# Kernel tuning notes

Measured on AMD Instinct MI355X. Metric: run time of the kernel, lower is better.

The kernel has to match this reference:

```python
import jax, jax.numpy as jnp
import numpy as np

N_HEADS = 16
HEAD_DIM = 64
D_MODEL = 1024

def setup_inputs() -> dict:
    key = jax.random.key(0)
    k1, k2, k3 = jax.random.split(key, 3)
    B, S = 4, 2048
    x = jax.random.normal(k1, (B, S, D_MODEL), dtype=jnp.float32)
    Wqkv = jax.random.normal(k2, (D_MODEL, 3 * D_MODEL), dtype=jnp.float32) * (D_MODEL ** -0.5)
    bqkv = jnp.zeros((3 * D_MODEL,), dtype=jnp.float32)
    Wo = jax.random.normal(k3, (D_MODEL, D_MODEL), dtype=jnp.float32) * (D_MODEL ** -0.5)
    bo = jnp.zeros((D_MODEL,), dtype=jnp.float32)
    return {"x": x, "Wqkv": Wqkv, "bqkv": bqkv, "Wo": Wo, "bo": bo}

def reference(x, Wqkv, bqkv, Wo, bo):
    B, S, E = x.shape
    H, D = N_HEADS, HEAD_DIM
    qkv = x @ Wqkv + bqkv                      # [B,S,3E]
    q, k, v = jnp.split(qkv, 3, axis=-1)
    q = q.reshape(B, S, H, D).transpose(0, 2, 1, 3)  # [B,H,S,D]
    k = k.reshape(B, S, H, D).transpose(0, 2, 1, 3)
    v = v.reshape(B, S, H, D).transpose(0, 2, 1, 3)
    scores = jnp.einsum('bhsd,bhtd->bhst', q, k) / jnp.sqrt(jnp.float32(D))
    causal = jnp.tril(jnp.ones((S, S), dtype=bool))
    scores = jnp.where(causal[None, None], scores, jnp.float32(-jnp.inf))
    attn = jax.nn.softmax(scores, axis=-1)
    y = jnp.einsum('bhst,bhtd->bhsd', attn, v)       # [B,H,S,D]
    y = y.transpose(0, 2, 1, 3).reshape(B, S, E)
    return y @ Wo + bo
```

## Files before the change

kernel.cpp:

```cpp
#include <hip/hip_runtime.h>
#include <hip/hip_bf16.h>
#include <stdint.h>

typedef __bf16 bf16;
typedef __bf16 bf16x8 __attribute__((ext_vector_type(8)));
typedef __bf16 bf16x4 __attribute__((ext_vector_type(4)));
typedef float  f32x4  __attribute__((ext_vector_type(4)));
typedef float  f32x16 __attribute__((ext_vector_type(16)));

__device__ __forceinline__ void load_lds16(const void* g, void* l) {
  __builtin_amdgcn_global_load_lds((const __attribute__((address_space(1))) void*)g,
                                   (__attribute__((address_space(3))) void*)l, 16, 0, 0);
}

__device__ __forceinline__ unsigned pk2(float a, float b) {
  union { bf16 h[2]; unsigned u; } t;
  t.h[0] = (bf16)a; t.h[1] = (bf16)b;
  return t.u;
}

__global__ __launch_bounds__(256) void f32_to_bf16_k(const float* __restrict__ in,
                                                     bf16* __restrict__ out) {
  int i = (blockIdx.x * 256 + threadIdx.x) * 8;
  float4 a = *(const float4*)(in + i);
  float4 b = *(const float4*)(in + i + 4);
  bf16x8 o;
  o[0] = (bf16)a.x; o[1] = (bf16)a.y; o[2] = (bf16)a.z; o[3] = (bf16)a.w;
  o[4] = (bf16)b.x; o[5] = (bf16)b.y; o[6] = (bf16)b.z; o[7] = (bf16)b.w;
  *(bf16x8*)(out + i) = o;
}

__global__ __launch_bounds__(256) void transpose_to_bf16_k(const float* __restrict__ in,
                                                           bf16* __restrict__ out,
                                                           int K, int N) {
  __shared__ __align__(16) bf16 tile[64 * 72];
  int n0 = blockIdx.x * 64, k0 = blockIdx.y * 64;
  int t = threadIdx.x;
  int r = t >> 2, cq = (t & 3) * 16;
  const float* src = in + (size_t)(k0 + r) * N + n0 + cq;
#pragma unroll
  for (int j = 0; j < 16; j += 4) {
    float4 v = *(const float4*)(src + j);
    tile[r * 72 + cq + j + 0] = (bf16)v.x;
    tile[r * 72 + cq + j + 1] = (bf16)v.y;
    tile[r * 72 + cq + j + 2] = (bf16)v.z;
    tile[r * 72 + cq + j + 3] = (bf16)v.w;
  }
  __syncthreads();
  bf16x8 r0, r1;
#pragma unroll
  for (int j = 0; j < 8; ++j) r0[j] = tile[(cq + j) * 72 + r];
#pragma unroll
  for (int j = 0; j < 8; ++j) r1[j] = tile[(cq + 8 + j) * 72 + r];
  bf16* dst = out + (size_t)(n0 + r) * K + k0 + cq;
  *(bf16x8*)(dst) = r0;
  *(bf16x8*)(dst + 8) = r1;
}

template <int EPI>
__global__ __launch_bounds__(256) void gemm_bt(const bf16* __restrict__ A,
                                               const bf16* __restrict__ BT,
                                               const float* __restrict__ bias,
                                               float* __restrict__ Cf,
                                               bf16* __restrict__ qk,
                                               bf16* __restrict__ vt,
                                               int M, int N, int K) {
  __shared__ __align__(16) bf16 As[128 * 64];
  __shared__ __align__(16) bf16 Bs[128 * 64];
  const int tid = threadIdx.x;
  const int w = tid >> 6, l = tid & 63;
  const int g = l >> 4, c = l & 15;
  const int wm = w >> 1, wn = w & 1;
  const int brow = blockIdx.y * 128;
  const int bcol = blockIdx.x * 128;
  const int lr = l >> 3;
  const int lg = l & 7;

  f32x4 acc[4][4];
#pragma unroll
  for (int m = 0; m < 4; ++m)
#pragma unroll
    for (int n = 0; n < 4; ++n) acc[m][n] = f32x4{0.f, 0.f, 0.f, 0.f};

  const int nkt = K >> 6;
  for (int kt = 0; kt < nkt; ++kt) {
    if (kt) __syncthreads();
    const int k0 = kt * 64;
#pragma unroll
    for (int i = 0; i < 4; ++i) {
      int row = w * 32 + i * 8 + lr;
      int src_k = k0 + ((lg ^ (row & 7)) * 8);
      load_lds16(A + (size_t)(brow + row) * K + src_k, &As[(w * 32 + i * 8) * 64]);
      load_lds16(BT + (size_t)(bcol + row) * K + src_k, &Bs[(w * 32 + i * 8) * 64]);
    }
    asm volatile("s_waitcnt vmcnt(0)" ::: "memory");
    __syncthreads();

#pragma unroll
    for (int ks = 0; ks < 2; ++ks) {
      bf16x8 af[4], bfr[4];
#pragma unroll
      for (int m = 0; m < 4; ++m)
        af[m] = *(const bf16x8*)&As[(wm * 64 + m * 16 + c) * 64 + (((ks * 4 + g) ^ (c & 7)) * 8)];
#pragma unroll
      for (int n = 0; n < 4; ++n)
        bfr[n] = *(const bf16x8*)&Bs[(wn * 64 + n * 16 + c) * 64 + (((ks * 4 + g) ^ (c & 7)) * 8)];
#pragma unroll
      for (int m = 0; m < 4; ++m)
#pragma unroll
        for (int n = 0; n < 4; ++n)
          acc[m][n] = __builtin_amdgcn_mfma_f32_16x16x32_bf16(af[m], bfr[n], acc[m][n], 0, 0, 0);
    }
  }

#pragma unroll
  for (int m = 0; m < 4; ++m) {
    int row_l = wm * 64 + m * 16 + (l >> 4) * 4;
#pragma unroll
    for (int n = 0; n < 4; ++n) {
      int col = bcol + wn * 64 + n * 16 + c;
      float bv = bias[col];
      if (EPI == 0) {
        if (bcol < 2048) {
#pragma unroll
          for (int r = 0; r < 4; ++r) {
            int row = brow + row_l + r;
            qk[(size_t)row * 2048 + col] = (bf16)(acc[m][n][r] + bv);
          }
        } else {
          int hh = (col - 2048) >> 6, dd = (col - 2048) & 63;
          int row0 = brow + row_l;
          int bb = row0 >> 11, ss = row0 & 2047;
          bf16x4 pk;
#pragma unroll
          for (int r = 0; r < 4; ++r) pk[r] = (bf16)(acc[m][n][r] + bv);
          *(bf16x4*)&vt[((size_t)(bb * 16 + hh) * 64 + dd) * 2048 + ss] = pk;
        }
      } else {
#pragma unroll
        for (int r = 0; r < 4; ++r) {
          int row = brow + row_l + r;
          Cf[(size_t)row * N + col] = acc[m][n][r] + bv;
        }
      }
    }
  }
}

__global__ __launch_bounds__(128) void attn_k(const bf16* __restrict__ qkbuf,
                                              const bf16* __restrict__ vtbuf,
                                              bf16* __restrict__ aout) {
  __shared__ __align__(16) bf16 Ks[2][64 * 64];
  __shared__ __align__(16) bf16 Vs[2][64 * 64];

  const int tid = threadIdx.x;
  const int w = tid >> 6, l = tid & 63;
  const int c32 = l & 31, hi = l >> 5;

  const int bid = blockIdx.x;
  const int xcd = bid & 7;
  const int idx = bid >> 3;
  const int bh = xcd * 8 + (idx >> 4);
  const int j = idx & 15;
  const int p = j >> 1, h0 = j & 1;
  const int b = bh >> 4, h = bh & 15;

  const bf16* ksrc = qkbuf + (size_t)(b * 2048) * 2048 + 1024 + h * 64;
  const bf16* vsrc = vtbuf + (size_t)(bh * 64) * 2048;

#pragma unroll 1
  for (int item = 0; item < 2; ++item) {
    const int qblk = item == 0 ? 15 - p : p;
    const int half = item == 0 ? h0 : 1 - h0;
    const int nt = 2 * qblk + half + 1;
    const int qw = qblk * 128 + half * 64 + w * 32;
    const int myq = qw + c32;

    const size_t qoff = (size_t)(b * 2048 + myq) * 2048 + h * 64;
    bf16x8 qf[4];
#pragma unroll
    for (int t = 0; t < 4; ++t) {
      bf16x8 v = *(const bf16x8*)&qkbuf[qoff + t * 16 + hi * 8];
#pragma unroll
      for (int jj = 0; jj < 8; ++jj) v[jj] = (bf16)((float)v[jj] * 0.125f);
      qf[t] = v;
    }

    float m_r = -1e30f, l_r = 0.f;
    f32x16 o[2];
    o[0] = (f32x16)(0.f); o[1] = (f32x16)(0.f);

#define STAGE_TILE(buf, KV0)                                                        \
    {                                                                               \
      const int kv0s = (KV0);                                                       \
      _Pragma("unroll")                                                             \
      for (int i = 0; i < 4; ++i) {                                                 \
        int rr = w * 32 + i * 8 + (l >> 3);                                         \
        int sw = ((l & 7) ^ (rr & 7)) * 8;                                          \
        load_lds16(ksrc + (size_t)(kv0s + rr) * 2048 + sw,                          \
                   &Ks[buf][(w * 32 + i * 8) * 64]);                                \
        load_lds16(vsrc + (size_t)rr * 2048 + kv0s + sw,                            \
                   &Vs[buf][(w * 32 + i * 8) * 64]);                                \
      }                                                                             \
    }

    STAGE_TILE(0, 0)
    asm volatile("s_waitcnt vmcnt(0)" ::: "memory");
    __syncthreads();

    int cur = 0;
    for (int kt = 0; kt < nt; ++kt) {
      const int kv0 = kt * 64;
      if (kt + 1 < nt) STAGE_TILE(cur ^ 1, kv0 + 64)

      const bf16* kb = &Ks[cur][0];
      const bf16* vb = &Vs[cur][0];

      f32x16 st[2];
      st[0] = (f32x16)(0.f); st[1] = (f32x16)(0.f);
      __builtin_amdgcn_s_setprio(1);
#pragma unroll
      for (int t = 0; t < 4; ++t) {
#pragma unroll
        for (int ks = 0; ks < 2; ++ks) {
          int kv = ks * 32 + c32;
          bf16x8 kf = *(const bf16x8*)&kb[kv * 64 + (((2 * t + hi) ^ (kv & 7)) * 8)];
          st[ks] = __builtin_amdgcn_mfma_f32_32x32x16_bf16(kf, qf[t], st[ks], 0, 0, 0);
        }
      }
      __builtin_amdgcn_s_setprio(0);

      if (kv0 + 63 > qw) {
#pragma unroll
        for (int ks = 0; ks < 2; ++ks)
#pragma unroll
          for (int r = 0; r < 16; ++r) {
            int kvidx = kv0 + ks * 32 + (r & 3) + 8 * (r >> 2) + 4 * hi;
            if (kvidx > myq) st[ks][r] = -1e30f;
          }
      }

      float t0[8];
#pragma unroll
      for (int i = 0; i < 8; ++i)
        t0[i] = fmaxf(fmaxf(st[0][i], st[0][i + 8]), fmaxf(st[1][i], st[1][i + 8]));
      float mx = fmaxf(fmaxf(fmaxf(t0[0], t0[1]), fmaxf(t0[2], t0[3])),
                       fmaxf(fmaxf(t0[4], t0[5]), fmaxf(t0[6], t0[7])));
      mx = fmaxf(mx, __shfl_xor(mx, 32, 64));

      if (__any(mx > m_r + 8.0f)) {
        float mn = fmaxf(m_r, mx);
        float al = __expf(m_r - mn);
        m_r = mn;
        l_r *= al;
#pragma unroll
        for (int ds = 0; ds < 2; ++ds)
#pragma unroll
          for (int r = 0; r < 16; ++r) o[ds][r] *= al;
      }

      float s0 = 0.f, s1 = 0.f, s2 = 0.f, s3 = 0.f;
#pragma unroll
      for (int ks = 0; ks < 2; ++ks)
#pragma unroll
        for (int r = 0; r < 16; r += 4) {
          float p0 = __expf(st[ks][r + 0] - m_r);
          float p1 = __expf(st[ks][r + 1] - m_r);
          float p2 = __expf(st[ks][r + 2] - m_r);
          float p3 = __expf(st[ks][r + 3] - m_r);
          st[ks][r + 0] = p0; st[ks][r + 1] = p1;
          st[ks][r + 2] = p2; st[ks][r + 3] = p3;
          s0 += p0; s1 += p1; s2 += p2; s3 += p3;
        }
      float ps = (s0 + s1) + (s2 + s3);
      ps += __shfl_xor(ps, 32, 64);
      l_r += ps;

      bf16x8 pfr[4];
#pragma unroll
      for (int t = 0; t < 4; ++t) {
        const int ks = t >> 1, eb = (t & 1) * 8;
        unsigned we0 = pk2(st[ks][eb + 0], st[ks][eb + 1]);
        unsigned we1 = pk2(st[ks][eb + 2], st[ks][eb + 3]);
        unsigned wo0 = pk2(st[ks][eb + 4], st[ks][eb + 5]);
        unsigned wo1 = pk2(st[ks][eb + 6], st[ks][eb + 7]);
        unsigned v0 = hi ? we0 : wo0;
        unsigned v1 = hi ? we1 : wo1;
        unsigned r0 = __shfl_xor(v0, 32, 64);
        unsigned r1 = __shfl_xor(v1, 32, 64);
        union { unsigned u[4]; bf16x8 v; } pf;
        pf.u[0] = hi ? r0 : we0;
        pf.u[1] = hi ? r1 : we1;
        pf.u[2] = hi ? wo0 : r0;
        pf.u[3] = hi ? wo1 : r1;
        pfr[t] = pf.v;
      }

      __builtin_amdgcn_s_setprio(1);
#pragma unroll
      for (int t = 0; t < 4; ++t) {
#pragma unroll
        for (int ds = 0; ds < 2; ++ds) {
          int d = ds * 32 + c32;
          bf16x8 vf = *(const bf16x8*)&vb[d * 64 + (((2 * t + hi) ^ (d & 7)) * 8)];
          o[ds] = __builtin_amdgcn_mfma_f32_32x32x16_bf16(vf, pfr[t], o[ds], 0, 0, 0);
        }
      }
      __builtin_amdgcn_s_setprio(0);

      asm volatile("s_waitcnt vmcnt(0)" ::: "memory");
      __syncthreads();
      cur ^= 1;
    }

    const float inv = 1.0f / l_r;
    bf16* orow = aout + (size_t)(b * 2048 + myq) * 1024 + h * 64;
#pragma unroll
    for (int ds = 0; ds < 2; ++ds)
#pragma unroll
      for (int rg = 0; rg < 4; ++rg) {
        bf16x4 pk;
#pragma unroll
        for (int i = 0; i < 4; ++i) pk[i] = (bf16)(o[ds][rg * 4 + i] * inv);
        *(bf16x4*)&orow[ds * 32 + rg * 8 + hi * 4] = pk;
      }
#undef STAGE_TILE
  }
}

extern "C" void kernel_launch(void* const* d_in, const int* in_sizes, int n_in,
                              void* d_out, int out_size, void* d_ws, size_t ws_size,
                              hipStream_t stream) {
  const float* x    = (const float*)d_in[0];
  const float* Wqkv = (const float*)d_in[1];
  const float* bqkv = (const float*)d_in[2];
  const float* Wo   = (const float*)d_in[3];
  const float* bo   = (const float*)d_in[4];
  float* out = (float*)d_out;

  char* ws = (char*)d_ws;
  bf16* xb   = (bf16*)(ws);
  bf16* wqt  = (bf16*)(ws + 16777216);
  bf16* wot  = (bf16*)(ws + 23068672);
  bf16* qkb  = (bf16*)(ws + 25165824);
  bf16* vtb  = (bf16*)(ws + 58720256);
  bf16* aob  = (bf16*)(ws + 75497472);

  f32_to_bf16_k<<<dim3(4096), dim3(256), 0, stream>>>(x, xb);
  transpose_to_bf16_k<<<dim3(48, 16), dim3(256), 0, stream>>>(Wqkv, wqt, 1024, 3072);
  transpose_to_bf16_k<<<dim3(16, 16), dim3(256), 0, stream>>>(Wo, wot, 1024, 1024);
  gemm_bt<0><<<dim3(24, 64), dim3(256), 0, stream>>>(xb, wqt, bqkv, nullptr, qkb, vtb,
                                                     8192, 3072, 1024);
  attn_k<<<dim3(1024), dim3(128), 0, stream>>>(qkb, vtb, aob);
  gemm_bt<1><<<dim3(8, 64), dim3(256), 0, stream>>>(aob, wot, bo, out, nullptr, nullptr,
                                                    8192, 1024, 1024);
}
```

Baseline: 194.2 us.

## Split attention into single-wave blocks per 32-query tile without double buffering

Rewrites the attention kernel so each 64-thread block (one wavefront) handles one 32-query tile. The launch goes from 1024 two-wave blocks, each processing two paired query blocks, to 4096 single-wave blocks ordered longest-first. Double-buffered LDS staging and __syncthreads are replaced by a single buffer loaded synchronously each iteration. This removes barriers, halves LDS per block and relies on many resident blocks for latency hiding. In exchange, each block reloads full K/V tiles alone, so K/V traffic per query doubles, and loads no longer overlap compute within a block.

New measurement: 221.1 us. +13.8%, slower.

```diff
diff --git a/kernel.cpp b/kernel.cpp
--- a/kernel.cpp
+++ b/kernel.cpp
@@ -147,185 +147,161 @@
   }
 }
 
-__global__ __launch_bounds__(128) void attn_k(const bf16* __restrict__ qkbuf,
-                                              const bf16* __restrict__ vtbuf,
-                                              bf16* __restrict__ aout) {
-  __shared__ __align__(16) bf16 Ks[2][64 * 64];
-  __shared__ __align__(16) bf16 Vs[2][64 * 64];
-
-  const int tid = threadIdx.x;
-  const int w = tid >> 6, l = tid & 63;
+__global__ __launch_bounds__(64) void attn_k(const bf16* __restrict__ qkbuf,
+                                             const bf16* __restrict__ vtbuf,
+                                             bf16* __restrict__ aout) {
+  __shared__ __align__(16) bf16 Ks[64 * 64];
+  __shared__ __align__(16) bf16 Vs[64 * 64];
+
+  const int l = threadIdx.x;
   const int c32 = l & 31, hi = l >> 5;
 
   const int bid = blockIdx.x;
   const int xcd = bid & 7;
-  const int idx = bid >> 3;
-  const int bh = xcd * 8 + (idx >> 4);
-  const int j = idx & 15;
-  const int p = j >> 1, h0 = j & 1;
+  const int u = bid >> 3;
+  const int bh = xcd * 8 + (u >> 6);
+  const int qb = 63 - (u & 63);
   const int b = bh >> 4, h = bh & 15;
+  const int q0 = qb * 32;
+  const int nt = (qb >> 1) + 1;
+  const int myq = q0 + c32;
 
   const bf16* ksrc = qkbuf + (size_t)(b * 2048) * 2048 + 1024 + h * 64;
   const bf16* vsrc = vtbuf + (size_t)(bh * 64) * 2048;
 
-#pragma unroll 1
-  for (int item = 0; item < 2; ++item) {
-    const int qblk = item == 0 ? 15 - p : p;
-    const int half = item == 0 ? h0 : 1 - h0;
-    const int nt = 2 * qblk + half + 1;
-    const int qw = qblk * 128 + half * 64 + w * 32;
-    const int myq = qw + c32;
-
-    const size_t qoff = (size_t)(b * 2048 + myq) * 2048 + h * 64;
-    bf16x8 qf[4];
+  const size_t qoff = (size_t)(b * 2048 + myq) * 2048 + h * 64;
+  bf16x8 qf[4];
+#pragma unroll
+  for (int t = 0; t < 4; ++t) {
+    bf16x8 v = *(const bf16x8*)&qkbuf[qoff + t * 16 + hi * 8];
+#pragma unroll
+    for (int j = 0; j < 8; ++j) v[j] = (bf16)((float)v[j] * 0.125f);
+    qf[t] = v;
+  }
+
+  float m_r = -1e30f, l_r = 0.f;
+  f32x16 o[2];
+  o[0] = (f32x16)(0.f); o[1] = (f32x16)(0.f);
+
+  for (int kt = 0; kt < nt; ++kt) {
+    const int kv0 = kt * 64;
+
+    asm volatile("s_waitcnt lgkmcnt(0)" ::: "memory");
+    __builtin_amdgcn_sched_barrier(0);
+#pragma unroll
+    for (int i = 0; i < 8; ++i) {
+      int row = i * 8 + (l >> 3);
+      int sw = ((l & 7) ^ (row & 7)) * 8;
+      load_lds16(ksrc + (size_t)(kv0 + row) * 2048 + sw, &Ks[(i * 8) * 64]);
+      load_lds16(vsrc + (size_t)row * 2048 + kv0 + sw, &Vs[(i * 8) * 64]);
+    }
+    asm volatile("s_waitcnt vmcnt(0)" ::: "memory");
+    __builtin_amdgcn_sched_barrier(0);
+
+    f32x16 st[2];
+    st[0] = (f32x16)(0.f); st[1] = (f32x16)(0.f);
+    __builtin_amdgcn_s_setprio(1);
 #pragma unroll
     for (int t = 0; t < 4; ++t) {
-      bf16x8 v = *(const bf16x8*)&qkbuf[qoff + t * 16 + hi * 8];
-#pragma unroll
-      for (int jj = 0; jj < 8; ++jj) v[jj] = (bf16)((float)v[jj] * 0.125f);
-      qf[t] = v;
-    }
-
-    float m_r = -1e30f, l_r = 0.f;
-    f32x16 o[2];
-    o[0] = (f32x16)(0.f); o[1] = (f32x16)(0.f);
-
-#define STAGE_TILE(buf, KV0)                                                        \
-    {                                                                               \
-      const int kv0s = (KV0);                                                       \
-      _Pragma("unroll")                                                             \
-      for (int i = 0; i < 4; ++i) {                                                 \
-        int rr = w * 32 + i * 8 + (l >> 3);                                         \
-        int sw = ((l & 7) ^ (rr & 7)) * 8;                                          \
-        load_lds16(ksrc + (size_t)(kv0s + rr) * 2048 + sw,                          \
-                   &Ks[buf][(w * 32 + i * 8) * 64]);                                \
-        load_lds16(vsrc + (size_t)rr * 2048 + kv0s + sw,                            \
-                   &Vs[buf][(w * 32 + i * 8) * 64]);                                \
-      }                                                                             \
-    }
-
-    STAGE_TILE(0, 0)
-    asm volatile("s_waitcnt vmcnt(0)" ::: "memory");
-    __syncthreads();
-
-    int cur = 0;
-    for (int kt = 0; kt < nt; ++kt) {
-      const int kv0 = kt * 64;
-      if (kt + 1 < nt) STAGE_TILE(cur ^ 1, kv0 + 64)
-
-      const bf16* kb = &Ks[cur][0];
-      const bf16* vb = &Vs[cur][0];
-
-      f32x16 st[2];
-      st[0] = (f32x16)(0.f); st[1] = (f32x16)(0.f);
-      __builtin_amdgcn_s_setprio(1);
-#pragma unroll
-      for (int t = 0; t < 4; ++t) {
-#pragma unroll
-        for (int ks = 0; ks < 2; ++ks) {
-          int kv = ks * 32 + c32;
-          bf16x8 kf = *(const bf16x8*)&kb[kv * 64 + (((2 * t + hi) ^ (kv & 7)) * 8)];
-          st[ks] = __builtin_amdgcn_mfma_f32_32x32x16_bf16(kf, qf[t], st[ks], 0, 0, 0);
+#pragma unroll
+      for (int ks = 0; ks < 2; ++ks) {
+        int kv = ks * 32 + c32;
+        bf16x8 kf = *(const bf16x8*)&Ks[kv * 64 + (((2 * t + hi) ^ (kv & 7)) * 8)];
+        st[ks] = __builtin_amdgcn_mfma_f32_32x32x16_bf16(kf, qf[t], st[ks], 0, 0, 0);
+      }
+    }
+    __builtin_amdgcn_s_setprio(0);
+
+    if (kv0 + 63 > q0) {
+#pragma unroll
+      for (int ks = 0; ks < 2; ++ks)
+#pragma unroll
+        for (int r = 0; r < 16; ++r) {
+          int kvidx = kv0 + ks * 32 + (r & 3) + 8 * (r >> 2) + 4 * hi;
+          if (kvidx > myq) st[ks][r] = -1e30f;
         }
+    }
+
+    float t0[8];
+#pragma unroll
+    for (int i = 0; i < 8; ++i)
+      t0[i] = fmaxf(fmaxf(st[0][i], st[0][i + 8]), fmaxf(st[1][i], st[1][i + 8]));
+    float mx = fmaxf(fmaxf(fmaxf(t0[0], t0[1]), fmaxf(t0[2], t0[3])),
+                     fmaxf(fmaxf(t0[4], t0[5]), fmaxf(t0[6], t0[7])));
+    mx = fmaxf(mx, __shfl_xor(mx, 32, 64));
+
+    if (__any(mx > m_r + 8.0f)) {
+      float mn = fmaxf(m_r, mx);
+      float al = __expf(m_r - mn);
+      m_r = mn;
+      l_r *= al;
+#pragma unroll
+      for (int ds = 0; ds < 2; ++ds)
+#pragma unroll
+        for (int r = 0; r < 16; ++r) o[ds][r] *= al;
+    }
+
+    float s0 = 0.f, s1 = 0.f, s2 = 0.f, s3 = 0.f;
+#pragma unroll
+    for (int ks = 0; ks < 2; ++ks)
+#pragma unroll
+      for (int r = 0; r < 16; r += 4) {
+        float p0 = __expf(st[ks][r + 0] - m_r);
+        float p1 = __expf(st[ks][r + 1] - m_r);
+        float p2 = __expf(st[ks][r + 2] - m_r);
+        float p3 = __expf(st[ks][r + 3] - m_r);
+        st[ks][r + 0] = p0; st[ks][r + 1] = p1;
+        st[ks][r + 2] = p2; st[ks][r + 3] = p3;
+        s0 += p0; s1 += p1; s2 += p2; s3 += p3;
       }
-      __builtin_amdgcn_s_setprio(0);
-
-      if (kv0 + 63 > qw) {
-#pragma unroll
-        for (int ks = 0; ks < 2; ++ks)
-#pragma unroll
-          for (int r = 0; r < 16; ++r) {
-            int kvidx = kv0 + ks * 32 + (r & 3) + 8 * (r >> 2) + 4 * hi;
-            if (kvidx > myq) st[ks][r] = -1e30f;
-          }
+    float ps = (s0 + s1) + (s2 + s3);
+    ps += __shfl_xor(ps, 32, 64);
+    l_r += ps;
+
+    bf16x8 pfr[4];
+#pragma unroll
+    for (int t = 0; t < 4; ++t) {
+      const int ks = t >> 1, eb = (t & 1) * 8;
+      unsigned we0 = pk2(st[ks][eb + 0], st[ks][eb + 1]);
+      unsigned we1 = pk2(st[ks][eb + 2], st[ks][eb + 3]);
+      unsigned wo0 = pk2(st[ks][eb + 4], st[ks][eb + 5]);
+      unsigned wo1 = pk2(st[ks][eb + 6], st[ks][eb + 7]);
+      unsigned v0 = hi ? we0 : wo0;
+      unsigned v1 = hi ? we1 : wo1;
+      unsigned r0 = __shfl_xor(v0, 32, 64);
+      unsigned r1 = __shfl_xor(v1, 32, 64);
+      union { unsigned u[4]; bf16x8 v; } pf;
+      pf.u[0] = hi ? r0 : we0;
+      pf.u[1] = hi ? r1 : we1;
+      pf.u[2] = hi ? wo0 : r0;
+      pf.u[3] = hi ? wo1 : r1;
+      pfr[t] = pf.v;
+    }
+
+    __builtin_amdgcn_s_setprio(1);
+#pragma unroll
+    for (int t = 0; t < 4; ++t) {
+#pragma unroll
+      for (int ds = 0; ds < 2; ++ds) {
+        int d = ds * 32 + c32;
+        bf16x8 vf = *(const bf16x8*)&Vs[d * 64 + (((2 * t + hi) ^ (d & 7)) * 8)];
+        o[ds] = __builtin_amdgcn_mfma_f32_32x32x16_bf16(vf, pfr[t], o[ds], 0, 0, 0);
       }
-
-      float t0[8];
-#pragma unroll
-      for (int i = 0; i < 8; ++i)
-        t0[i] = fmaxf(fmaxf(st[0][i], st[0][i + 8]), fmaxf(st[1][i], st[1][i + 8]));
-      float mx = fmaxf(fmaxf(fmaxf(t0[0], t0[1]), fmaxf(t0[2], t0[3])),
-                       fmaxf(fmaxf(t0[4], t0[5]), fmaxf(t0[6], t0[7])));
-      mx = fmaxf(mx, __shfl_xor(mx, 32, 64));
-
-      if (__any(mx > m_r + 8.0f)) {
-        float mn = fmaxf(m_r, mx);
-        float al = __expf(m_r - mn);
-        m_r = mn;
-        l_r *= al;
-#pragma unroll
-        for (int ds = 0; ds < 2; ++ds)
-#pragma unroll
-          for (int r = 0; r < 16; ++r) o[ds][r] *= al;
-      }
-
-      float s0 = 0.f, s1 = 0.f, s2 = 0.f, s3 = 0.f;
-#pragma unroll
-      for (int ks = 0; ks < 2; ++ks)
-#pragma unroll
-        for (int r = 0; r < 16; r += 4) {
-          float p0 = __expf(st[ks][r + 0] - m_r);
-          float p1 = __expf(st[ks][r + 1] - m_r);
-          float p2 = __expf(st[ks][r + 2] - m_r);
-          float p3 = __expf(st[ks][r + 3] - m_r);
-          st[ks][r + 0] = p0; st[ks][r + 1] = p1;
-          st[ks][r + 2] = p2; st[ks][r + 3] = p3;
-          s0 += p0; s1 += p1; s2 += p2; s3 += p3;
-        }
-      float ps = (s0 + s1) + (s2 + s3);
-      ps += __shfl_xor(ps, 32, 64);
-      l_r += ps;
-
-      bf16x8 pfr[4];
-#pragma unroll
-      for (int t = 0; t < 4; ++t) {
-        const int ks = t >> 1, eb = (t & 1) * 8;
-        unsigned we0 = pk2(st[ks][eb + 0], st[ks][eb + 1]);
-        unsigned we1 = pk2(st[ks][eb + 2], st[ks][eb + 3]);
-        unsigned wo0 = pk2(st[ks][eb + 4], st[ks][eb + 5]);
-        unsigned wo1 = pk2(st[ks][eb + 6], st[ks][eb + 7]);
-        unsigned v0 = hi ? we0 : wo0;
-        unsigned v1 = hi ? we1 : wo1;
-        unsigned r0 = __shfl_xor(v0, 32, 64);
-        unsigned r1 = __shfl_xor(v1, 32, 64);
-        union { unsigned u[4]; bf16x8 v; } pf;
-        pf.u[0] = hi ? r0 : we0;
-        pf.u[1] = hi ? r1 : we1;
-        pf.u[2] = hi ? wo0 : r0;
-        pf.u[3] = hi ? wo1 : r1;
-        pfr[t] = pf.v;
-      }
-
-      __builtin_amdgcn_s_setprio(1);
-#pragma unroll
-      for (int t = 0; t < 4; ++t) {
-#pragma unroll
-        for (int ds = 0; ds < 2; ++ds) {
-          int d = ds * 32 + c32;
-          bf16x8 vf = *(const bf16x8*)&vb[d * 64 + (((2 * t + hi) ^ (d & 7)) * 8)];
-          o[ds] = __builtin_amdgcn_mfma_f32_32x32x16_bf16(vf, pfr[t], o[ds], 0, 0, 0);
-        }
-      }
-      __builtin_amdgcn_s_setprio(0);
-
-      asm volatile("s_waitcnt vmcnt(0)" ::: "memory");
-      __syncthreads();
-      cur ^= 1;
-    }
-
-    const float inv = 1.0f / l_r;
-    bf16* orow = aout + (size_t)(b * 2048 + myq) * 1024 + h * 64;
-#pragma unroll
-    for (int ds = 0; ds < 2; ++ds)
-#pragma unroll
-      for (int rg = 0; rg < 4; ++rg) {
-        bf16x4 pk;
-#pragma unroll
-        for (int i = 0; i < 4; ++i) pk[i] = (bf16)(o[ds][rg * 4 + i] * inv);
-        *(bf16x4*)&orow[ds * 32 + rg * 8 + hi * 4] = pk;
-      }
-#undef STAGE_TILE
-  }
+    }
+    __builtin_amdgcn_s_setprio(0);
+  }
+
+  const float inv = 1.0f / l_r;
+  bf16* orow = aout + (size_t)(b * 2048 + myq) * 1024 + h * 64;
+#pragma unroll
+  for (int ds = 0; ds < 2; ++ds)
+#pragma unroll
+    for (int rg = 0; rg < 4; ++rg) {
+      bf16x4 pk;
+#pragma unroll
+      for (int i = 0; i < 4; ++i) pk[i] = (bf16)(o[ds][rg * 4 + i] * inv);
+      *(bf16x4*)&orow[ds * 32 + rg * 8 + hi * 4] = pk;
+    }
 }
 
 extern "C" void kernel_launch(void* const* d_in, const int* in_sizes, int n_in,
@@ -351,7 +327,7 @@
   transpose_to_bf16_k<<<dim3(16, 16), dim3(256), 0, stream>>>(Wo, wot, 1024, 1024);
   gemm_bt<0><<<dim3(24, 64), dim3(256), 0, stream>>>(xb, wqt, bqkv, nullptr, qkb, vtb,
                                                      8192, 3072, 1024);
-  attn_k<<<dim3(1024), dim3(128), 0, stream>>>(qkb, vtb, aob);
+  attn_k<<<dim3(4096), dim3(64), 0, stream>>>(qkb, vtb, aob);
   gemm_bt<1><<<dim3(8, 64), dim3(256), 0, stream>>>(aob, wot, bo, out, nullptr, nullptr,
                                                     8192, 1024, 1024);
 }
```

## Use permlane32_swap for cross-half exchange and MFMA-based softmax row sums

Applied to the files above, without the earlier changes.

Replaces the __shfl_xor lane exchanges (ds_bpermute through LDS) with the gfx950 permlane32_swap intrinsic for the row max and for packing P into MFMA operand layout. It also drops the scalar VALU accumulation of the softmax denominator and computes it with an extra MFMA against a vector of ones, so the sum comes from the bf16-rounded P. This is meant to cut VALU and LDS-permute work in the inner attention loop. In exchange it adds one more MFMA per sub-tile and an extra 16-register accumulator, which raises register pressure.

New measurement: 219.6 us. 13.1% more time.

```diff
diff --git a/kernel.cpp b/kernel.cpp
--- a/kernel.cpp
+++ b/kernel.cpp
@@ -7,6 +7,7 @@
 typedef __bf16 bf16x4 __attribute__((ext_vector_type(4)));
 typedef float  f32x4  __attribute__((ext_vector_type(4)));
 typedef float  f32x16 __attribute__((ext_vector_type(16)));
+typedef unsigned u32x2 __attribute__((ext_vector_type(2)));
 
 __device__ __forceinline__ void load_lds16(const void* g, void* l) {
   __builtin_amdgcn_global_load_lds((const __attribute__((address_space(1))) void*)g,
@@ -168,6 +169,11 @@
   const bf16* ksrc = qkbuf + (size_t)(b * 2048) * 2048 + 1024 + h * 64;
   const bf16* vsrc = vtbuf + (size_t)(bh * 64) * 2048;
 
+  union { unsigned u[4]; bf16x8 v; } one_;
+  one_.u[0] = 0x3F803F80u; one_.u[1] = 0x3F803F80u;
+  one_.u[2] = 0x3F803F80u; one_.u[3] = 0x3F803F80u;
+  const bf16x8 ones = one_.v;
+
 #pragma unroll 1
   for (int item = 0; item < 2; ++item) {
     const int qblk = item == 0 ? 15 - p : p;
@@ -186,9 +192,9 @@
       qf[t] = v;
     }
 
-    float m_r = -1e30f, l_r = 0.f;
-    f32x16 o[2];
-    o[0] = (f32x16)(0.f); o[1] = (f32x16)(0.f);
+    float m_r = -1e30f;
+    f32x16 o[2], osum;
+    o[0] = (f32x16)(0.f); o[1] = (f32x16)(0.f); osum = (f32x16)(0.f);
 
 #define STAGE_TILE(buf, KV0)                                                        \
     {                                                                               \
@@ -246,53 +252,41 @@
         t0[i] = fmaxf(fmaxf(st[0][i], st[0][i + 8]), fmaxf(st[1][i], st[1][i + 8]));
       float mx = fmaxf(fmaxf(fmaxf(t0[0], t0[1]), fmaxf(t0[2], t0[3])),
                        fmaxf(fmaxf(t0[4], t0[5]), fmaxf(t0[6], t0[7])));
-      mx = fmaxf(mx, __shfl_xor(mx, 32, 64));
+      {
+        u32x2 mres = __builtin_amdgcn_permlane32_swap(__float_as_uint(mx),
+                                                      __float_as_uint(mx), false, false);
+        mx = fmaxf(__uint_as_float(mres[0]), __uint_as_float(mres[1]));
+      }
 
       if (__any(mx > m_r + 8.0f)) {
         float mn = fmaxf(m_r, mx);
         float al = __expf(m_r - mn);
         m_r = mn;
-        l_r *= al;
 #pragma unroll
         for (int ds = 0; ds < 2; ++ds)
 #pragma unroll
           for (int r = 0; r < 16; ++r) o[ds][r] *= al;
-      }
-
-      float s0 = 0.f, s1 = 0.f, s2 = 0.f, s3 = 0.f;
+#pragma unroll
+        for (int r = 0; r < 16; ++r) osum[r] *= al;
+      }
+
 #pragma unroll
       for (int ks = 0; ks < 2; ++ks)
 #pragma unroll
-        for (int r = 0; r < 16; r += 4) {
-          float p0 = __expf(st[ks][r + 0] - m_r);
-          float p1 = __expf(st[ks][r + 1] - m_r);
-          float p2 = __expf(st[ks][r + 2] - m_r);
-          float p3 = __expf(st[ks][r + 3] - m_r);
-          st[ks][r + 0] = p0; st[ks][r + 1] = p1;
-          st[ks][r + 2] = p2; st[ks][r + 3] = p3;
-          s0 += p0; s1 += p1; s2 += p2; s3 += p3;
-        }
-      float ps = (s0 + s1) + (s2 + s3);
-      ps += __shfl_xor(ps, 32, 64);
-      l_r += ps;
+        for (int r = 0; r < 16; ++r) st[ks][r] = __expf(st[ks][r] - m_r);
 
       bf16x8 pfr[4];
 #pragma unroll
       for (int t = 0; t < 4; ++t) {
         const int ks = t >> 1, eb = (t & 1) * 8;
-        unsigned we0 = pk2(st[ks][eb + 0], st[ks][eb + 1]);
-        unsigned we1 = pk2(st[ks][eb + 2], st[ks][eb + 3]);
-        unsigned wo0 = pk2(st[ks][eb + 4], st[ks][eb + 5]);
-        unsigned wo1 = pk2(st[ks][eb + 6], st[ks][eb + 7]);
-        unsigned v0 = hi ? we0 : wo0;
-        unsigned v1 = hi ? we1 : wo1;
-        unsigned r0 = __shfl_xor(v0, 32, 64);
-        unsigned r1 = __shfl_xor(v1, 32, 64);
+        unsigned w0 = pk2(st[ks][eb + 0], st[ks][eb + 1]);
+        unsigned w1 = pk2(st[ks][eb + 2], st[ks][eb + 3]);
+        unsigned w2 = pk2(st[ks][eb + 4], st[ks][eb + 5]);
+        unsigned w3 = pk2(st[ks][eb + 6], st[ks][eb + 7]);
+        u32x2 r02 = __builtin_amdgcn_permlane32_swap(w0, w2, false, false);
+        u32x2 r13 = __builtin_amdgcn_permlane32_swap(w1, w3, false, false);
         union { unsigned u[4]; bf16x8 v; } pf;
-        pf.u[0] = hi ? r0 : we0;
-        pf.u[1] = hi ? r1 : we1;
-        pf.u[2] = hi ? wo0 : r0;
-        pf.u[3] = hi ? wo1 : r1;
+        pf.u[0] = r02[0]; pf.u[1] = r13[0]; pf.u[2] = r02[1]; pf.u[3] = r13[1];
         pfr[t] = pf.v;
       }
 
@@ -305,6 +299,7 @@
           bf16x8 vf = *(const bf16x8*)&vb[d * 64 + (((2 * t + hi) ^ (d & 7)) * 8)];
           o[ds] = __builtin_amdgcn_mfma_f32_32x32x16_bf16(vf, pfr[t], o[ds], 0, 0, 0);
         }
+        osum = __builtin_amdgcn_mfma_f32_32x32x16_bf16(ones, pfr[t], osum, 0, 0, 0);
       }
       __builtin_amdgcn_s_setprio(0);
 
@@ -313,7 +308,7 @@
       cur ^= 1;
     }
 
-    const float inv = 1.0f / l_r;
+    const float inv = 1.0f / osum[0];
     bf16* orow = aout + (size_t)(b * 2048 + myq) * 1024 + h * 64;
 #pragma unroll
     for (int ds = 0; ds < 2; ++ds)
```
